# Performance work log

Hardware: AMD Instinct MI355X
Metric: run time of the kernel (lower is better)

## Reference

```python
import jax, jax.numpy as jnp
import numpy as np

B, N, IN_DIM, D, H, L = 8, 256, 2, 128, 512, 2
EPS = 1e-5


def layer_norm(x, g, b):
    m = jnp.mean(x, axis=-1, keepdims=True)
    v = jnp.var(x, axis=-1, keepdims=True)
    return (x - m) * jax.lax.rsqrt(v + EPS) * g + b


def loo_max_pool(nodes):
    # nodes: (B, N, D) -> leave-one-out max over the set axis -> (B, N, D)
    n = nodes.shape[1]
    neg = jnp.finfo(nodes.dtype).min
    mask = jnp.eye(n, dtype=bool)[None, :, :, None]          # (1, N, N, 1)
    expanded = jnp.broadcast_to(nodes[:, None, :, :],
                                (nodes.shape[0], n, n, nodes.shape[2]))
    return jnp.where(mask, neg, expanded).max(axis=2)        # (B, N, D)


def setup_inputs() -> dict:
    key = jax.random.key(0)
    ks = jax.random.split(key, 16)
    s = 0.02
    inp = {
        "x":   jax.random.normal(ks[0], (B, N, IN_DIM), dtype=jnp.float32),
        # embedding linear + its LayerNorm
        "We":  jax.random.normal(ks[1], (IN_DIM, D)) * s,
        "be":  jnp.zeros((D,), jnp.float32),
        "ge":  jnp.ones((D,), jnp.float32),
        "bge": jnp.zeros((D,), jnp.float32),
        # per-layer pool linear (concat of x and LOO-pooled context: 2D -> D)
        "Wp":  jax.random.normal(ks[2], (L, 2 * D, D)) * s,
        "bp":  jnp.zeros((L, D), jnp.float32),
        "gp":  jnp.ones((L, D), jnp.float32),
        "bgp": jnp.zeros((L, D), jnp.float32),
        # per-layer feed-forward D -> H -> D
        "W1":  jax.random.normal(ks[3], (L, D, H)) * s,
        "b1":  jnp.zeros((L, H), jnp.float32),
        "W2":  jax.random.normal(ks[4], (L, H, D)) * s,
        "b2":  jnp.zeros((L, D), jnp.float32),
        "gf":  jnp.ones((L, D), jnp.float32),
        "bgf": jnp.zeros((L, D), jnp.float32),
    }
    return inp


def reference(x, We, be, ge, bge, Wp, bp, gp, bgp, W1, b1, W2, b2, gf, bgf):
    # embeddings + embedding norm
    h = layer_norm(x @ We + be, ge, bge)                      # (B, N, D)
    for i in range(L):
        # pool layer: LOO max pooling, concat, linear, residual, norm
        pooled = loo_max_pool(h)                              # (B, N, D)
        cat = jnp.concatenate([h, pooled], axis=-1)           # (B, N, 2D)
        h = layer_norm(h + cat @ Wp[i] + bp[i], gp[i], bgp[i])
        # feed-forward, residual, norm
        ff = jax.nn.relu(h @ W1[i] + b1[i]) @ W2[i] + b2[i]
        h = layer_norm(h + ff, gf[i], bgf[i])
    return h
```

## Files before the change

kernel.cpp:

```cpp
#include <hip/hip_runtime.h>
#include <hip/hip_bf16.h>

#define BB 8
#define NN 256
#define DD 128
#define HH 512
#define LL 2
#define EPSV 1e-5f
#define TPB 8
#define BPL (NN/TPB)

typedef unsigned short ushort_t;
typedef __attribute__((ext_vector_type(8))) short bf16x8;
typedef __attribute__((ext_vector_type(4))) float f32x4;

#define WPSZ (256*128)
#define W1SZ (128*512)
#define W2SZ (512*128)
#define LAYSZ (WPSZ+W1SZ+W2SZ)
#define TOTW (2*LAYSZ)

__device__ __forceinline__ ushort_t f2b(float v){
  __hip_bfloat16 h = __float2bfloat16(v);
  return *(ushort_t*)&h;
}

__device__ __forceinline__ void waveRed2(float &a, float &b){
  #pragma unroll
  for (int off=32; off>=1; off>>=1){
    a += __shfl_xor(a, off, 64);
    b += __shfl_xor(b, off, 64);
  }
}

__device__ __forceinline__ void poolMerge(float &m1, float &m2, int &am,
                                          float o1, float o2, int oa){
  if (o1 > m1){ m2 = fmaxf(m1, o2); m1 = o1; am = oa; }
  else        { m2 = fmaxf(m2, o1); }
}

__global__ __launch_bounds__(512) void k_prep(
    const float* __restrict__ Wp, const float* __restrict__ W1,
    const float* __restrict__ W2, ushort_t* __restrict__ wcvt)
{
  int e8 = blockIdx.x*512 + threadIdx.x;
  if (e8 >= TOTW/8) return;
  int e = e8*8;
  int l2 = (e >= LAYSZ) ? 1 : 0;
  int el = e - l2*LAYSZ;
  const float* src; int N, KSlog, off;
  if (el < WPSZ)           { src = Wp + (size_t)l2*WPSZ; N = 128; KSlog = 3; off = el; }
  else if (el < WPSZ+W1SZ) { src = W1 + (size_t)l2*W1SZ; N = 512; KSlog = 2; off = el - WPSZ; }
  else                     { src = W2 + (size_t)l2*W2SZ; N = 128; KSlog = 4; off = el - (WPSZ+W1SZ); }
  int rec  = off >> 9;
  int ln   = (off >> 3) & 63;
  int n0t  = rec >> KSlog;
  int ks   = rec & ((1<<KSlog)-1);
  int row0 = ks*32 + ((ln>>4)<<3);
  int col  = (n0t<<4) + (ln&15);
  bf16x8 v;
  #pragma unroll
  for (int j=0;j<8;++j) v[j] = (short)f2b(src[(size_t)(row0+j)*N + col]);
  *(bf16x8*)(wcvt + e) = v;
}

__global__ __launch_bounds__(512, 2) void k_net(
    int layer,
    const float* __restrict__ x, const float* __restrict__ We,
    const float* __restrict__ be, const float* __restrict__ ge,
    const float* __restrict__ bge,
    float* __restrict__ hio,
    float* __restrict__ pm1, float* __restrict__ pm2, int* __restrict__ pma,
    const ushort_t* __restrict__ wL,
    const float* __restrict__ bp,
    const float* __restrict__ gp, const float* __restrict__ bgp,
    const float* __restrict__ b1,
    const float* __restrict__ b2,
    const float* __restrict__ gf, const float* __restrict__ bgf)
{
  int tid = threadIdx.x;
  int d = tid & 127, fourth = tid >> 7;
  int wv = tid >> 6;
  int lane = tid & 63;
  int m = lane & 15, q = lane >> 4;
  int t0 = blockIdx.x * TPB;
  int b = t0 >> 8;
  int blk = (t0 >> 3) & (BPL-1);
  int n0a = wv*16;

  const ushort_t* wAb = wL;
  const ushort_t* wBb = wL + WPSZ;
  const ushort_t* wCb = wL + WPSZ + W1SZ;

  __shared__ float    hcur[8*128];
  __shared__ ushort_t catb[16*256];
  __shared__ float    sA[16*128];
  __shared__ ushort_t h1b[16*128];
  __shared__ float    h1f[8*128];
  __shared__ ushort_t ub[16*512];
  __shared__ float fm1[128], fm2[128];
  __shared__ int   fam[128];
  __shared__ float sm1[4][128], sm2[4][128];
  __shared__ int   sam[4][128];
  __shared__ float xs[512];
  __shared__ float red9[2][12];
  __shared__ float stats[12];

  if (layer == 0){
    xs[tid] = x[(size_t)b*512 + tid];
    float a = We[d], bw = We[128+d], c = be[d];
    if (fourth == 0){
      float r0=a, r1=bw;        waveRed2(r0,r1);
      float r2=c, r3=a*a;       waveRed2(r2,r3);
      float r4=bw*bw, r5=c*c;   waveRed2(r4,r5);
      float r6=a*bw, r7=a*c;    waveRed2(r6,r7);
      float r8=bw*c, r9=0.f;    waveRed2(r8,r9);
      int w = (tid >> 6) & 1;
      if (lane == 0){
        red9[w][0]=r0; red9[w][1]=r1; red9[w][2]=r2; red9[w][3]=r3;
        red9[w][4]=r4; red9[w][5]=r5; red9[w][6]=r6; red9[w][7]=r7;
        red9[w][8]=r8;
      }
    }
    __syncthreads();
    if (tid < 9) stats[tid] = (red9[0][tid] + red9[1][tid]) * (1.f/128);
    __syncthreads();
    float mA=stats[0], mB=stats[1], mC=stats[2];
    float SAA=stats[3], SBB=stats[4], SCC=stats[5];
    float SAB=stats[6], SAC=stats[7], SBC=stats[8];
    float gev = ge[d], bgev = bge[d];
    float m1=-3.4e38f, m2=-3.4e38f; int am=0;
    for (int i=0;i<64;++i){
      int n = fourth*64 + i;
      float x0 = xs[2*n], x1 = xs[2*n+1];
      float v    = fmaf(x0, a,  fmaf(x1, bw, c));
      float mean = fmaf(x0, mA, fmaf(x1, mB, mC));
      float ev2  = x0*x0*SAA + x1*x1*SBB + SCC
                 + 2.f*(x0*x1*SAB + x0*SAC + x1*SBC);
      float var = ev2 - mean*mean;
      float hv = (v-mean)*rsqrtf(var+EPSV)*gev + bgev;
      poolMerge(m1,m2,am, hv, -3.4e38f, n);
    }
    sm1[fourth][d]=m1; sm2[fourth][d]=m2; sam[fourth][d]=am;
    #pragma unroll
    for (int rep=0; rep<2; ++rep){
      int t = fourth*2 + rep;
      int n = (t0 & 255) + t;
      float x0 = xs[2*n], x1 = xs[2*n+1];
      float v    = fmaf(x0, a,  fmaf(x1, bw, c));
      float mean = fmaf(x0, mA, fmaf(x1, mB, mC));
      float ev2  = x0*x0*SAA + x1*x1*SBB + SCC
                 + 2.f*(x0*x1*SAB + x0*SAC + x1*SBC);
      float var = ev2 - mean*mean;
      hcur[t*128 + d] = (v-mean)*rsqrtf(var+EPSV)*gev + bgev;
    }
    __syncthreads();
  } else {
    {
      size_t base = ((size_t)b*BPL + fourth*8)*128 + d;
      float m1 = pm1[base], m2 = pm2[base]; int am = pma[base];
      #pragma unroll
      for (int i=1;i<8;++i)
        poolMerge(m1,m2,am, pm1[base+(size_t)i*128], pm2[base+(size_t)i*128],
                  pma[base+(size_t)i*128]);
      sm1[fourth][d]=m1; sm2[fourth][d]=m2; sam[fourth][d]=am;
    }
    #pragma unroll
    for (int rep=0; rep<2; ++rep){
      int t = fourth*2 + rep;
      hcur[t*128 + d] = hio[(size_t)(t0+t)*DD + d];
    }
    __syncthreads();
  }

  if (fourth==0){
    float m1=sm1[0][d], m2=sm2[0][d]; int am=sam[0][d];
    #pragma unroll
    for (int p=1;p<4;++p) poolMerge(m1,m2,am, sm1[p][d], sm2[p][d], sam[p][d]);
    fm1[d]=m1; fm2[d]=m2; fam[d]=am;
  }
  __syncthreads();

  #pragma unroll
  for (int rep=0; rep<4; ++rep){
    int e = rep*512 + tid;
    int t = e >> 8, cc = e & 255;
    int n = (t0 & 255) + t;
    float v;
    if (cc < DD) v = hcur[t*128 + cc];
    else { int c2 = cc - DD; v = (n==fam[c2]) ? fm2[c2] : fm1[c2]; }
    *(ushort_t*)((char*)catb + ((e*2) ^ ((t&7)<<4))) = f2b(v);
  }
  __syncthreads();

  {
    f32x4 acc = {0.f,0.f,0.f,0.f};
    const char* apb = (const char*)catb;
    int abase = (m*256 + q*8)*2;
    int sw = (m&7)<<4;
    #pragma unroll
    for (int ks=0; ks<8; ++ks){
      bf16x8 wf = *(const bf16x8*)(wAb + ((size_t)(wv*8+ks)*64 + lane)*8);
      bf16x8 af = *(const bf16x8*)(apb + ((abase + ks*64) ^ sw));
      acc = __builtin_amdgcn_mfma_f32_16x16x32_bf16(af, wf, acc, 0,0,0);
    }
    #pragma unroll
    for (int r=0;r<4;++r) sA[(q*4+r)*128 + n0a + m] = acc[r];
  }
  __syncthreads();

  {
    int t = wv, g = lane;
    float2 v2 = *(const float2*)&sA[t*128 + 2*g];
    float v0 = v2.x + bp[2*g]   + hcur[t*128 + 2*g];
    float v1 = v2.y + bp[2*g+1] + hcur[t*128 + 2*g + 1];
    float s = v0+v1, qq = v0*v0 + v1*v1;
    waveRed2(s,qq);
    float mean = s*(1.f/128), var = qq*(1.f/128) - mean*mean;
    float rs = rsqrtf(var + EPSV);
    float o0 = (v0-mean)*rs*gp[2*g]   + bgp[2*g];
    float o1 = (v1-mean)*rs*gp[2*g+1] + bgp[2*g+1];
    unsigned pk = (unsigned)f2b(o0) | ((unsigned)f2b(o1) << 16);
    *(unsigned*)((char*)h1b + (((t*128 + 2*g)*2) ^ ((t&7)<<4))) = pk;
    *(float2*)&h1f[t*128 + 2*g] = make_float2(o0, o1);
  }
  __syncthreads();

  {
    const char* apb = (const char*)h1b;
    int abase = (m*128 + q*8)*2;
    int sw = (m&7)<<4;
    bf16x8 af[4];
    #pragma unroll
    for (int ks=0; ks<4; ++ks)
      af[ks] = *(const bf16x8*)(apb + ((abase + ks*64) ^ sw));
    #pragma unroll
    for (int half=0; half<2; ++half){
      #pragma unroll
      for (int i=0;i<2;++i){
        int n0 = (half*2+i)*128 + wv*16;
        int n0t = (half*2+i)*8 + wv;
        f32x4 acc = {0.f,0.f,0.f,0.f};
        #pragma unroll
        for (int ks=0; ks<4; ++ks){
          bf16x8 wf = *(const bf16x8*)(wBb + ((size_t)(n0t*4+ks)*64 + lane)*8);
          acc = __builtin_amdgcn_mfma_f32_16x16x32_bf16(af[ks], wf, acc, 0,0,0);
        }
        float bb = b1[n0+m];
        #pragma unroll
        for (int r=0;r<4;++r){
          int row = q*4+r;
          *(ushort_t*)((char*)ub + (((row*512 + n0 + m)*2) ^ ((row&7)<<4)))
              = f2b(fmaxf(acc[r] + bb, 0.f));
        }
      }
    }
  }
  __syncthreads();

  {
    f32x4 acc = {0.f,0.f,0.f,0.f};
    const char* apb = (const char*)ub;
    int abase = (m*512 + q*8)*2;
    int sw = (m&7)<<4;
    #pragma unroll
    for (int kk=0; kk<16; ++kk){
      bf16x8 wf = *(const bf16x8*)(wCb + ((size_t)(wv*16+kk)*64 + lane)*8);
      bf16x8 af = *(const bf16x8*)(apb + ((abase + kk*64) ^ sw));
      acc = __builtin_amdgcn_mfma_f32_16x16x32_bf16(af, wf, acc, 0,0,0);
    }
    #pragma unroll
    for (int r=0;r<4;++r) sA[(q*4+r)*128 + n0a + m] = acc[r];
  }
  __syncthreads();

  {
    int t = wv, g = lane;
    float2 v2 = *(const float2*)&sA[t*128 + 2*g];
    float v0 = v2.x + b2[2*g]   + h1f[t*128 + 2*g];
    float v1 = v2.y + b2[2*g+1] + h1f[t*128 + 2*g + 1];
    float s = v0+v1, qq = v0*v0 + v1*v1;
    waveRed2(s,qq);
    float mean = s*(1.f/128), var = qq*(1.f/128) - mean*mean;
    float rs = rsqrtf(var + EPSV);
    float o0 = (v0-mean)*rs*gf[2*g]   + bgf[2*g];
    float o1 = (v1-mean)*rs*gf[2*g+1] + bgf[2*g+1];
    *(float2*)&hio[(size_t)(t0+t)*DD + 2*g] = make_float2(o0, o1);
    *(float2*)&hcur[t*128 + 2*g] = make_float2(o0, o1);
  }
  if (layer == 0){
    __syncthreads();
    if (tid < 128){
      int n0 = t0 & 255;
      float m1 = hcur[tid], m2 = -3.4e38f; int am = n0;
      #pragma unroll
      for (int p=1;p<TPB;++p)
        poolMerge(m1,m2,am, hcur[p*128+tid], -3.4e38f, n0+p);
      size_t idx = ((size_t)b*BPL + blk)*128 + tid;
      pm1[idx]=m1; pm2[idx]=m2; pma[idx]=am;
    }
  }
}

extern "C" void kernel_launch(void* const* d_in, const int* in_sizes, int n_in,
                              void* d_out, int out_size, void* d_ws, size_t ws_size,
                              hipStream_t stream)
{
  const float* x   = (const float*)d_in[0];
  const float* We  = (const float*)d_in[1];
  const float* be  = (const float*)d_in[2];
  const float* ge  = (const float*)d_in[3];
  const float* bge = (const float*)d_in[4];
  const float* Wp  = (const float*)d_in[5];
  const float* bp  = (const float*)d_in[6];
  const float* gp  = (const float*)d_in[7];
  const float* bgp = (const float*)d_in[8];
  const float* W1  = (const float*)d_in[9];
  const float* b1  = (const float*)d_in[10];
  const float* W2  = (const float*)d_in[11];
  const float* b2  = (const float*)d_in[12];
  const float* gf  = (const float*)d_in[13];
  const float* bgf = (const float*)d_in[14];

  float* hio = (float*)d_out;
  char* ws = (char*)d_ws;
  const size_t NP = (size_t)BB*BPL*128;
  float* p1 = (float*)ws;            ws += NP*4;
  float* p2 = (float*)ws;            ws += NP*4;
  int*   pa = (int*)ws;              ws += NP*4;
  ushort_t* wcvt = (ushort_t*)ws;

  const int grid = (BB*NN)/TPB;

  k_prep<<<80, 512, 0, stream>>>(Wp, W1, W2, wcvt);

  k_net<<<grid, 512, 0, stream>>>(0, x, We, be, ge, bge, hio, p1, p2, pa,
      wcvt,
      bp,      gp,      bgp,
      b1,      b2,
      gf,      bgf);

  k_net<<<grid, 512, 0, stream>>>(1, x, We, be, ge, bge, hio, p1, p2, pa,
      wcvt + LAYSZ,
      bp + DD, gp + DD, bgp + DD,
      b1 + HH, b2 + DD,
      gf + DD, bgf + DD);
}
```

Baseline: 108.4 us.

## Prefetch MFMA weight fragments into registers early and precompute layer-0 norm stats

Weight fragments for the pool and first FFN GEMMs are loaded into registers at kernel start, and the second FFN weights are loaded right after the pool GEMM. A scheduling barrier keeps these loads hoisted so global latency overlaps the pooling and layernorm phases. Layer 0 also computes per-token mean/rstd once into shared memory instead of recomputing them per channel. The first half of the concat buffer is written while loading h. The cost is many more live VGPRs (about 40 bf16x8 vectors), which can lower occupancy or cause spills.

```diff
diff --git a/kernel.cpp b/kernel.cpp
--- a/kernel.cpp
+++ b/kernel.cpp
@@ -19,6 +19,15 @@
 #define W2SZ (512*128)
 #define LAYSZ (WPSZ+W1SZ+W2SZ)
 #define TOTW (2*LAYSZ)
+
+#if defined(__has_builtin)
+#if __has_builtin(__builtin_amdgcn_sched_barrier)
+#define SCHED_FENCE() __builtin_amdgcn_sched_barrier(0)
+#endif
+#endif
+#ifndef SCHED_FENCE
+#define SCHED_FENCE()
+#endif
 
 __device__ __forceinline__ ushort_t f2b(float v){
   __hip_bfloat16 h = __float2bfloat16(v);
@@ -92,6 +101,15 @@
   const ushort_t* wBb = wL + WPSZ;
   const ushort_t* wCb = wL + WPSZ + W1SZ;
 
+  bf16x8 wfa[8], wfb[16];
+  #pragma unroll
+  for (int ks=0; ks<8; ++ks)
+    wfa[ks] = *(const bf16x8*)(wAb + ((size_t)(wv*8+ks)*64 + lane)*8);
+  #pragma unroll
+  for (int r=0; r<16; ++r)
+    wfb[r] = *(const bf16x8*)(wBb + ((size_t)(((r>>2)*8+wv)*4 + (r&3))*64 + lane)*8);
+  SCHED_FENCE();
+
   __shared__ float    hcur[8*128];
   __shared__ ushort_t catb[16*256];
   __shared__ float    sA[16*128];
@@ -105,6 +123,7 @@
   __shared__ float xs[512];
   __shared__ float red9[2][12];
   __shared__ float stats[12];
+  __shared__ float4 tk[256];
 
   if (layer == 0){
     xs[tid] = x[(size_t)b*512 + tid];
@@ -125,20 +144,25 @@
     __syncthreads();
     if (tid < 9) stats[tid] = (red9[0][tid] + red9[1][tid]) * (1.f/128);
     __syncthreads();
-    float mA=stats[0], mB=stats[1], mC=stats[2];
-    float SAA=stats[3], SBB=stats[4], SCC=stats[5];
-    float SAB=stats[6], SAC=stats[7], SBC=stats[8];
+    if (tid < 256){
+      float mA=stats[0], mB=stats[1], mC=stats[2];
+      float SAA=stats[3], SBB=stats[4], SCC=stats[5];
+      float SAB=stats[6], SAC=stats[7], SBC=stats[8];
+      float x0 = xs[2*tid], x1 = xs[2*tid+1];
+      float mean = fmaf(x0, mA, fmaf(x1, mB, mC));
+      float ev2  = x0*x0*SAA + x1*x1*SBB + SCC
+                 + 2.f*(x0*x1*SAB + x0*SAC + x1*SBC);
+      float var = ev2 - mean*mean;
+      tk[tid] = make_float4(x0, x1, mean, rsqrtf(var + EPSV));
+    }
+    __syncthreads();
     float gev = ge[d], bgev = bge[d];
     float m1=-3.4e38f, m2=-3.4e38f; int am=0;
     for (int i=0;i<64;++i){
       int n = fourth*64 + i;
-      float x0 = xs[2*n], x1 = xs[2*n+1];
-      float v    = fmaf(x0, a,  fmaf(x1, bw, c));
-      float mean = fmaf(x0, mA, fmaf(x1, mB, mC));
-      float ev2  = x0*x0*SAA + x1*x1*SBB + SCC
-                 + 2.f*(x0*x1*SAB + x0*SAC + x1*SBC);
-      float var = ev2 - mean*mean;
-      float hv = (v-mean)*rsqrtf(var+EPSV)*gev + bgev;
+      float4 t4 = tk[n];
+      float v  = fmaf(t4.x, a, fmaf(t4.y, bw, c));
+      float hv = fmaf((v - t4.z)*t4.w, gev, bgev);
       poolMerge(m1,m2,am, hv, -3.4e38f, n);
     }
     sm1[fourth][d]=m1; sm2[fourth][d]=m2; sam[fourth][d]=am;
@@ -146,13 +170,11 @@
     for (int rep=0; rep<2; ++rep){
       int t = fourth*2 + rep;
       int n = (t0 & 255) + t;
-      float x0 = xs[2*n], x1 = xs[2*n+1];
-      float v    = fmaf(x0, a,  fmaf(x1, bw, c));
-      float mean = fmaf(x0, mA, fmaf(x1, mB, mC));
-      float ev2  = x0*x0*SAA + x1*x1*SBB + SCC
-                 + 2.f*(x0*x1*SAB + x0*SAC + x1*SBC);
-      float var = ev2 - mean*mean;
-      hcur[t*128 + d] = (v-mean)*rsqrtf(var+EPSV)*gev + bgev;
+      float4 t4 = tk[n];
+      float v  = fmaf(t4.x, a, fmaf(t4.y, bw, c));
+      float hv = fmaf((v - t4.z)*t4.w, gev, bgev);
+      hcur[t*128 + d] = hv;
+      *(ushort_t*)((char*)catb + (((t*256 + d)*2) ^ ((t&7)<<4))) = f2b(hv);
     }
     __syncthreads();
   } else {
@@ -168,7 +190,9 @@
     #pragma unroll
     for (int rep=0; rep<2; ++rep){
       int t = fourth*2 + rep;
-      hcur[t*128 + d] = hio[(size_t)(t0+t)*DD + d];
+      float hv = hio[(size_t)(t0+t)*DD + d];
+      hcur[t*128 + d] = hv;
+      *(ushort_t*)((char*)catb + (((t*256 + d)*2) ^ ((t&7)<<4))) = f2b(hv);
     }
     __syncthreads();
   }
@@ -182,14 +206,12 @@
   __syncthreads();
 
   #pragma unroll
-  for (int rep=0; rep<4; ++rep){
+  for (int rep=0; rep<2; ++rep){
     int e = rep*512 + tid;
-    int t = e >> 8, cc = e & 255;
+    int t = e >> 7, c2 = e & 127;
     int n = (t0 & 255) + t;
-    float v;
-    if (cc < DD) v = hcur[t*128 + cc];
-    else { int c2 = cc - DD; v = (n==fam[c2]) ? fm2[c2] : fm1[c2]; }
-    *(ushort_t*)((char*)catb + ((e*2) ^ ((t&7)<<4))) = f2b(v);
+    float v = (n==fam[c2]) ? fm2[c2] : fm1[c2];
+    *(ushort_t*)((char*)catb + (((t*256 + 128 + c2)*2) ^ ((t&7)<<4))) = f2b(v);
   }
   __syncthreads();
 
@@ -200,13 +222,17 @@
     int sw = (m&7)<<4;
     #pragma unroll
     for (int ks=0; ks<8; ++ks){
-      bf16x8 wf = *(const bf16x8*)(wAb + ((size_t)(wv*8+ks)*64 + lane)*8);
       bf16x8 af = *(const bf16x8*)(apb + ((abase + ks*64) ^ sw));
-      acc = __builtin_amdgcn_mfma_f32_16x16x32_bf16(af, wf, acc, 0,0,0);
+      acc = __builtin_amdgcn_mfma_f32_16x16x32_bf16(af, wfa[ks], acc, 0,0,0);
     }
     #pragma unroll
     for (int r=0;r<4;++r) sA[(q*4+r)*128 + n0a + m] = acc[r];
   }
+  bf16x8 wfc[16];
+  #pragma unroll
+  for (int kk=0; kk<16; ++kk)
+    wfc[kk] = *(const bf16x8*)(wCb + ((size_t)(wv*16+kk)*64 + lane)*8);
+  SCHED_FENCE();
   __syncthreads();
 
   {
@@ -238,14 +264,12 @@
     for (int half=0; half<2; ++half){
       #pragma unroll
       for (int i=0;i<2;++i){
-        int n0 = (half*2+i)*128 + wv*16;
-        int n0t = (half*2+i)*8 + wv;
+        int idx4 = half*2+i;
+        int n0 = idx4*128 + wv*16;
         f32x4 acc = {0.f,0.f,0.f,0.f};
         #pragma unroll
-        for (int ks=0; ks<4; ++ks){
-          bf16x8 wf = *(const bf16x8*)(wBb + ((size_t)(n0t*4+ks)*64 + lane)*8);
-          acc = __builtin_amdgcn_mfma_f32_16x16x32_bf16(af[ks], wf, acc, 0,0,0);
-        }
+        for (int ks=0; ks<4; ++ks)
+          acc = __builtin_amdgcn_mfma_f32_16x16x32_bf16(af[ks], wfb[idx4*4+ks], acc, 0,0,0);
         float bb = b1[n0+m];
         #pragma unroll
         for (int r=0;r<4;++r){
@@ -265,9 +289,8 @@
     int sw = (m&7)<<4;
     #pragma unroll
     for (int kk=0; kk<16; ++kk){
-      bf16x8 wf = *(const bf16x8*)(wCb + ((size_t)(wv*16+kk)*64 + lane)*8);
       bf16x8 af = *(const bf16x8*)(apb + ((abase + kk*64) ^ sw));
-      acc = __builtin_amdgcn_mfma_f32_16x16x32_bf16(af, wf, acc, 0,0,0);
+      acc = __builtin_amdgcn_mfma_f32_16x16x32_bf16(af, wfc[kk], acc, 0,0,0);
     }
     #pragma unroll
     for (int r=0;r<4;++r) sA[(q*4+r)*128 + n0a + m] = acc[r];
```

New measurement: 103.6 us. -4.4%, faster.
